# Kernel tuning notes

Measured on AMD Instinct MI355X. Metric: run time of the kernel, lower is better.

The kernel has to match this reference:

```python
import jax, jax.numpy as jnp
import numpy as np

H, D = 4, 8          # heads, per-head dim (hidden=32)
HID = 32
NA = 300_000         # addr nodes
NT = 300_000         # tx nodes
E_IN, E_OUT, E_SP = 1_000_000, 1_000_000, 500_000
NLAYERS = 4
NREL = 3


def setup_inputs() -> dict:
    key = jax.random.key(0)
    ks = iter(jax.random.split(key, 40))
    s = 0.1
    inp = {}
    inp['x_addr'] = jax.random.normal(next(ks), (NA, 53), jnp.float32)
    inp['x_tx'] = jax.random.normal(next(ks), (NT, 6), jnp.float32)
    inp['ei_input'] = jax.random.randint(next(ks), (2, E_IN), 0, NA, jnp.int32)   # addr -> tx
    inp['ei_output'] = jax.random.randint(next(ks), (2, E_OUT), 0, NT, jnp.int32)  # tx -> addr
    inp['ei_spent'] = jax.random.randint(next(ks), (2, E_SP), 0, NT, jnp.int32)   # tx -> tx
    # node encoders
    inp['enc_w_addr'] = jax.random.normal(next(ks), (53, HID), jnp.float32) * s
    inp['enc_b_addr'] = jnp.zeros((HID,), jnp.float32)
    inp['enc_w_tx'] = jax.random.normal(next(ks), (6, HID), jnp.float32) * s
    inp['enc_b_tx'] = jnp.zeros((HID,), jnp.float32)
    # layer norms (shared across layers as in the source)
    inp['ln_addr_g'] = jnp.ones((HID,), jnp.float32)
    inp['ln_addr_b'] = jnp.zeros((HID,), jnp.float32)
    inp['ln_tx_g'] = jnp.ones((HID,), jnp.float32)
    inp['ln_tx_b'] = jnp.zeros((HID,), jnp.float32)
    # 4 HANConv layers, params stacked on leading layer axis
    inp['proj_w_addr'] = jax.random.normal(next(ks), (NLAYERS, HID, HID), jnp.float32) * s
    inp['proj_b_addr'] = jnp.zeros((NLAYERS, HID), jnp.float32)
    inp['proj_w_tx'] = jax.random.normal(next(ks), (NLAYERS, HID, HID), jnp.float32) * s
    inp['proj_b_tx'] = jnp.zeros((NLAYERS, HID), jnp.float32)
    inp['att_src'] = jax.random.normal(next(ks), (NLAYERS, NREL, H, D), jnp.float32) * s
    inp['att_dst'] = jax.random.normal(next(ks), (NLAYERS, NREL, H, D), jnp.float32) * s
    inp['klin_w'] = jax.random.normal(next(ks), (NLAYERS, HID, HID), jnp.float32) * s
    inp['klin_b'] = jnp.zeros((NLAYERS, HID), jnp.float32)
    inp['q'] = jax.random.normal(next(ks), (NLAYERS, HID), jnp.float32) * s
    # output head
    inp['lin_w'] = jax.random.normal(next(ks), (HID, 2), jnp.float32) * s
    inp['lin_b'] = jnp.zeros((2,), jnp.float32)
    return inp


def _layernorm(x, g, b, eps=1e-5):
    m = x.mean(-1, keepdims=True)
    v = ((x - m) ** 2).mean(-1, keepdims=True)
    return (x - m) / jnp.sqrt(v + eps) * g + b


def _segment_softmax(alpha, idx, n):
    # alpha: [E, H]; numerically stable softmax over ragged segments (dst nodes)
    amax = jax.ops.segment_max(alpha, idx, num_segments=n)
    amax = jnp.where(jnp.isfinite(amax), amax, 0.0)
    ex = jnp.exp(alpha - amax[idx])
    den = jax.ops.segment_sum(ex, idx, num_segments=n)
    return ex / (den[idx] + 1e-16)


def _han_conv(xa, xt, ei_in, ei_out, ei_sp,
              pw_a, pb_a, pw_t, pb_t, a_src, a_dst, kw, kb, q):
    h_a = (xa @ pw_a + pb_a).reshape(-1, H, D)   # [NA,H,D]
    h_t = (xt @ pw_t + pb_t).reshape(-1, H, D)   # [NT,H,D]
    rels = [(h_a, h_t, ei_in, 0, 'tx'),     # ('addr','input','tx')
            (h_t, h_a, ei_out, 1, 'addr'),  # ('tx','output','addr')
            (h_t, h_t, ei_sp, 2, 'tx')]     # ('tx','spent_output','tx')
    outs = {'addr': [], 'tx': []}
    for hs, hd, ei, t, dname in rels:
        asrc = (hs * a_src[t]).sum(-1)   # [Ns,H]
        adst = (hd * a_dst[t]).sum(-1)   # [Nd,H]
        si, di = ei[0], ei[1]
        e = jax.nn.leaky_relu(asrc[si] + adst[di], negative_slope=0.2)  # [E,H]
        w = _segment_softmax(e, di, hd.shape[0])                        # [E,H]
        msg = hs[si] * w[:, :, None]                                    # [E,H,D]
        agg = jax.ops.segment_sum(msg, di, num_segments=hd.shape[0])
        outs[dname].append(jax.nn.relu(agg.reshape(-1, H * D)))
    def group(xs):
        out = jnp.stack(xs)                                   # [R,N,F]
        score = (q * jnp.tanh(out @ kw + kb).mean(1)).sum(-1)  # [R]
        attn = jax.nn.softmax(score)
        return (attn[:, None, None] * out).sum(0)
    return group(outs['addr']), group(outs['tx'])


def reference(x_addr, x_tx, ei_input, ei_output, ei_spent,
              enc_w_addr, enc_b_addr, enc_w_tx, enc_b_tx,
              ln_addr_g, ln_addr_b, ln_tx_g, ln_tx_b,
              proj_w_addr, proj_b_addr, proj_w_tx, proj_b_tx,
              att_src, att_dst, klin_w, klin_b, q,
              lin_w, lin_b):
    xa = jax.nn.relu(x_addr @ enc_w_addr + enc_b_addr)
    xt = jax.nn.relu(x_tx @ enc_w_tx + enc_b_tx)
    for l in range(NLAYERS):
        oa, ot = _han_conv(xa, xt, ei_input, ei_output, ei_spent,
                           proj_w_addr[l], proj_b_addr[l],
                           proj_w_tx[l], proj_b_tx[l],
                           att_src[l], att_dst[l],
                           klin_w[l], klin_b[l], q[l])
        xa = _layernorm(jax.nn.relu(oa) + xa, ln_addr_g, ln_addr_b)
        xt = _layernorm(jax.nn.relu(ot) + xt, ln_tx_g, ln_tx_b)
    return xa @ lin_w + lin_b
```

## Files before the change

### kernel.cpp

```cpp
#include <hip/hip_runtime.h>
#include <hip/hip_fp16.h>

#define NLAYERS 4
#define BSHIFT 10
#define CHUNK 4096

typedef _Float16 f16x8 __attribute__((ext_vector_type(8)));
typedef float f32x4 __attribute__((ext_vector_type(4)));

__global__ void zero_int_kernel(int* __restrict__ p, long n) {
    long i = (long)blockIdx.x * 256 + threadIdx.x;
    long stride = (long)gridDim.x * 256;
    for (; i < n; i += stride) p[i] = 0;
}

__device__ __forceinline__ float fast_tanh(float y) {
    y = fminf(fmaxf(y, -15.f), 15.f);
    float t = __expf(2.f * y);
    return (t - 1.f) / (t + 1.f);
}

__device__ __forceinline__ int edge_row(const int* ei_in, const int* ei_out, const int* ei_sp,
                                        int E_IN, int E_OUT, int E_SP, int NT, int NA,
                                        int e, int* src) {
    if (e < E_IN) { *src = ei_in[e]; return ei_in[E_IN + e]; }
    if (e < E_IN + E_OUT) { int i = e - E_IN; *src = ei_out[i]; return NT + ei_out[E_OUT + i]; }
    int i = e - E_IN - E_OUT; *src = ei_sp[i]; return NT + NA + ei_sp[E_SP + i];
}

__global__ void hist_kernel(const int* __restrict__ ei_in, const int* __restrict__ ei_out,
                            const int* __restrict__ ei_sp, int E_IN, int E_OUT, int E_SP,
                            int NT, int NA, int* __restrict__ deg, int E_TOT) {
    int e = blockIdx.x * 256 + threadIdx.x;
    if (e >= E_TOT) return;
    int s;
    int row = edge_row(ei_in, ei_out, ei_sp, E_IN, E_OUT, E_SP, NT, NA, e, &s);
    atomicAdd(&deg[row], 1);
}

__global__ void scatter_kernel(const int* __restrict__ ei_in, const int* __restrict__ ei_out,
                               const int* __restrict__ ei_sp, int E_IN, int E_OUT, int E_SP,
                               int NT, int NA, int* __restrict__ cursor, int* __restrict__ col,
                               int E_TOT) {
    int e = blockIdx.x * 256 + threadIdx.x;
    if (e >= E_TOT) return;
    int s;
    int row = edge_row(ei_in, ei_out, ei_sp, E_IN, E_OUT, E_SP, NT, NA, e, &s);
    int pos = atomicAdd(&cursor[row], 1);
    col[pos] = s;
}

__global__ void scan1_kernel(const int* __restrict__ deg, int* __restrict__ rowptr,
                             int* __restrict__ bsum, int n) {
    __shared__ int lds[256];
    int tid = threadIdx.x;
    int base = blockIdx.x * 1024;
    int v[4];
    int mysum = 0;
    #pragma unroll
    for (int j = 0; j < 4; j++) {
        int idx = base + tid * 4 + j;
        v[j] = (idx < n) ? deg[idx] : 0;
        mysum += v[j];
    }
    lds[tid] = mysum;
    __syncthreads();
    for (int off = 1; off < 256; off <<= 1) {
        int t = (tid >= off) ? lds[tid - off] : 0;
        __syncthreads();
        lds[tid] += t;
        __syncthreads();
    }
    int excl = lds[tid] - mysum;
    if (tid == 255) bsum[blockIdx.x] = lds[tid];
    int run = excl;
    #pragma unroll
    for (int j = 0; j < 4; j++) {
        int idx = base + tid * 4 + j;
        if (idx < n) rowptr[idx] = run;
        run += v[j];
    }
}

__global__ void scan2_kernel(int* __restrict__ bsum, int nb) {
    __shared__ int lds[1024];
    int tid = threadIdx.x;
    int v = (tid < nb) ? bsum[tid] : 0;
    lds[tid] = v;
    __syncthreads();
    for (int off = 1; off < 1024; off <<= 1) {
        int t = (tid >= off) ? lds[tid - off] : 0;
        __syncthreads();
        lds[tid] += t;
        __syncthreads();
    }
    if (tid < nb) bsum[tid] = lds[tid] - v;
}

__global__ void scan3_kernel(int* __restrict__ rowptr, const int* __restrict__ bsum,
                             int* __restrict__ cursor, int n, int E) {
    int i = blockIdx.x * 256 + threadIdx.x;
    if (i < n) {
        int r = rowptr[i] + bsum[i >> 10];
        rowptr[i] = r;
        cursor[i] = r;
    }
    if (i == 0) rowptr[n] = E;
}

__global__ void bucket_scatter_kernel(const int* __restrict__ ei_in, const int* __restrict__ ei_out,
                                      const int* __restrict__ ei_sp, int E_IN, int E_OUT, int E_SP,
                                      int NT, int NA, int* __restrict__ bcur,
                                      uint2* __restrict__ ebuf, int E_TOT, int nbuck, int cap) {
    __shared__ int lc[1024], lbase[1024], lcur[1024];
    int tid = threadIdx.x;
    int chunk0 = blockIdx.x * CHUNK;
    int chunkN = E_TOT - chunk0;
    if (chunkN > CHUNK) chunkN = CHUNK;
    if (chunkN <= 0) return;
    for (int i = tid; i < nbuck; i += 256) { lc[i] = 0; lcur[i] = 0; }
    __syncthreads();
    for (int i = tid; i < chunkN; i += 256) {
        int s;
        int row = edge_row(ei_in, ei_out, ei_sp, E_IN, E_OUT, E_SP, NT, NA, chunk0 + i, &s);
        atomicAdd(&lc[row >> BSHIFT], 1);
    }
    __syncthreads();
    for (int i = tid; i < nbuck; i += 256) if (lc[i]) lbase[i] = atomicAdd(&bcur[i], lc[i]);
    __syncthreads();
    for (int i = tid; i < chunkN; i += 256) {
        int s;
        int row = edge_row(ei_in, ei_out, ei_sp, E_IN, E_OUT, E_SP, NT, NA, chunk0 + i, &s);
        int b = row >> BSHIFT;
        int pos = lbase[b] + atomicAdd(&lcur[b], 1);
        if (pos < cap) ebuf[(size_t)b * cap + pos] = make_uint2((unsigned)row, (unsigned)s);
    }
}

__global__ void scanb_kernel(const int* __restrict__ bcur, int* __restrict__ boff,
                             int* __restrict__ rowptr, int nbuck, int cap, int NCAT) {
    __shared__ int lds[1024];
    int tid = threadIdx.x;
    int v = 0;
    if (tid < nbuck) { v = bcur[tid]; if (v > cap) v = cap; }
    lds[tid] = v;
    __syncthreads();
    for (int off = 1; off < 1024; off <<= 1) {
        int t = (tid >= off) ? lds[tid - off] : 0;
        __syncthreads();
        lds[tid] += t;
        __syncthreads();
    }
    if (tid < nbuck) boff[tid] = lds[tid] - v;
    if (tid == 1023) {
        boff[nbuck] = lds[1023];
        rowptr[NCAT] = lds[1023];
    }
}

__global__ void __launch_bounds__(256) bucket_csr_kernel(
    const uint2* __restrict__ ebuf, const int* __restrict__ boff,
    int* __restrict__ rowptr, int* __restrict__ col, int NCAT, int cap) {
    __shared__ int ldeg[1024];
    __shared__ int lsum[256];
    int tid = threadIdx.x;
    int b = blockIdx.x;
    int row0 = b << BSHIFT;
    int e0 = boff[b], e1 = boff[b + 1];
    int cnt = e1 - e0;
    const uint2* src = ebuf + (size_t)b * cap;
    for (int i = tid; i < 1024; i += 256) ldeg[i] = 0;
    __syncthreads();
    for (int i = tid; i < cnt; i += 256)
        atomicAdd(&ldeg[src[i].x - (unsigned)row0], 1);
    __syncthreads();
    int bidx = tid * 4;
    int v0 = ldeg[bidx], v1 = ldeg[bidx + 1], v2 = ldeg[bidx + 2], v3 = ldeg[bidx + 3];
    int mysum = v0 + v1 + v2 + v3;
    lsum[tid] = mysum;
    __syncthreads();
    for (int off = 1; off < 256; off <<= 1) {
        int t = (tid >= off) ? lsum[tid - off] : 0;
        __syncthreads();
        lsum[tid] += t;
        __syncthreads();
    }
    int run = e0 + lsum[tid] - mysum;
    int vv[4] = {v0, v1, v2, v3};
    #pragma unroll
    for (int j = 0; j < 4; j++) {
        int r = bidx + j;
        if (row0 + r < NCAT) rowptr[row0 + r] = run;
        ldeg[r] = run;
        run += vv[j];
    }
    __syncthreads();
    for (int i = tid; i < cnt; i += 256) {
        uint2 p = src[i];
        int pos = atomicAdd(&ldeg[p.x - (unsigned)row0], 1);
        col[pos] = (int)p.y;
    }
}

__global__ void __launch_bounds__(256) encproj_addr_kernel(
    const float* __restrict__ x,
    const float* __restrict__ We, const float* __restrict__ be,
    const float* __restrict__ Wp, const float* __restrict__ bp,
    const float* __restrict__ a0, const float* __restrict__ a1,
    float* __restrict__ xa, __half* __restrict__ h,
    __half* __restrict__ o0, float* __restrict__ o1,
    int n, int gpb) {
    __shared__ __align__(16) float lds_t[4][16][36];
    __shared__ float sx[4][16 * 57];
    int tid = threadIdx.x;
    int wave = tid >> 6, lane = tid & 63;
    int colid = lane & 15, kgrp = lane >> 4;
    int fbase = kgrp * 8;

    f16x8 bE00, bE01, bE10, bE11;
    #pragma unroll
    for (int j = 0; j < 8; j++) {
        int k0 = fbase + j;
        int k1 = 32 + fbase + j;
        bE00[j] = (_Float16)We[k0 * 32 + colid];
        bE01[j] = (_Float16)We[k0 * 32 + 16 + colid];
        float w10 = (k1 < 53) ? We[k1 * 32 + colid] : 0.f;
        float w11 = (k1 < 53) ? We[k1 * 32 + 16 + colid] : 0.f;
        bE10[j] = (_Float16)w10;
        bE11[j] = (_Float16)w11;
    }
    float beC0 = be[colid], beC1 = be[16 + colid];

    f16x8 bP0, bP1;
    #pragma unroll
    for (int j = 0; j < 8; j++) {
        bP0[j] = (_Float16)Wp[(fbase + j) * 32 + colid];
        bP1[j] = (_Float16)Wp[(fbase + j) * 32 + 16 + colid];
    }
    float bpC0 = bp[colid], bpC1 = bp[16 + colid];

    float va0[8], va1[8];
    #pragma unroll
    for (int j = 0; j < 8; j++) { va0[j] = a0[fbase + j]; va1[j] = a1[fbase + j]; }

    float (*tp)[36] = lds_t[wave];
    float* sxw = sx[wave];
    int blockBase = blockIdx.x * gpb * 64;
    for (int gi = 0; gi < gpb; gi++) {
        int node0 = blockBase + gi * 64 + wave * 16;
        int node = node0 + colid;
        bool valid = node < n;
        int nn = n - node0;
        if (nn > 16) nn = 16;
        if (nn < 0) nn = 0;
        int elems = nn * 53;
        for (int i = lane; i < elems; i += 64) {
            int r = i / 53, c = i - r * 53;
            sxw[r * 57 + c] = x[(size_t)node0 * 53 + i];
        }
        f16x8 af0, af1;
        #pragma unroll
        for (int j = 0; j < 8; j++) {
            af0[j] = (_Float16)sxw[colid * 57 + fbase + j];
            int kk = 32 + fbase + j;
            float v1 = (kk < 53) ? sxw[colid * 57 + kk] : 0.f;
            af1[j] = (_Float16)v1;
        }
        f32x4 c0 = {0.f, 0.f, 0.f, 0.f};
        f32x4 c1 = {0.f, 0.f, 0.f, 0.f};
        c0 = __builtin_amdgcn_mfma_f32_16x16x32_f16(af0, bE00, c0, 0, 0, 0);
        c0 = __builtin_amdgcn_mfma_f32_16x16x32_f16(af1, bE10, c0, 0, 0, 0);
        c1 = __builtin_amdgcn_mfma_f32_16x16x32_f16(af0, bE01, c1, 0, 0, 0);
        c1 = __builtin_amdgcn_mfma_f32_16x16x32_f16(af1, bE11, c1, 0, 0, 0);
        #pragma unroll
        for (int r = 0; r < 4; r++) {
            c0[r] = fmaxf(c0[r] + beC0, 0.f);
            c1[r] = fmaxf(c1[r] + beC1, 0.f);
        }
        #pragma unroll
        for (int r = 0; r < 4; r++) {
            int row = kgrp * 4 + r;
            tp[row][colid] = c0[r];
            tp[row][16 + colid] = c1[r];
        }
        float4 xlo = *(const float4*)&tp[colid][fbase];
        float4 xhi = *(const float4*)&tp[colid][fbase + 4];
        float xe[8] = {xlo.x, xlo.y, xlo.z, xlo.w, xhi.x, xhi.y, xhi.z, xhi.w};
        if (valid) {
            size_t basep = (size_t)node * 32 + fbase;
            *(float4*)(xa + basep) = xlo;
            *(float4*)(xa + basep + 4) = xhi;
        }
        f16x8 af;
        #pragma unroll
        for (int j = 0; j < 8; j++) af[j] = (_Float16)xe[j];
        f32x4 p0 = {0.f, 0.f, 0.f, 0.f};
        f32x4 p1 = {0.f, 0.f, 0.f, 0.f};
        p0 = __builtin_amdgcn_mfma_f32_16x16x32_f16(af, bP0, p0, 0, 0, 0);
        p1 = __builtin_amdgcn_mfma_f32_16x16x32_f16(af, bP1, p1, 0, 0, 0);
        #pragma unroll
        for (int r = 0; r < 4; r++) { p0[r] += bpC0; p1[r] += bpC1; }
        #pragma unroll
        for (int r = 0; r < 4; r++) {
            int row = kgrp * 4 + r;
            tp[row][colid] = p0[r];
            tp[row][16 + colid] = p1[r];
        }
        float4 hlo = *(const float4*)&tp[colid][fbase];
        float4 hhi = *(const float4*)&tp[colid][fbase + 4];
        float hv[8] = {hlo.x, hlo.y, hlo.z, hlo.w, hhi.x, hhi.y, hhi.z, hhi.w};
        if (valid) {
            float4 hout;
            __half2* hp2 = (__half2*)&hout;
            hp2[0] = __floats2half2_rn(hv[0], hv[1]);
            hp2[1] = __floats2half2_rn(hv[2], hv[3]);
            hp2[2] = __floats2half2_rn(hv[4], hv[5]);
            hp2[3] = __floats2half2_rn(hv[6], hv[7]);
            *(float4*)(h + (size_t)node * 32 + fbase) = hout;
            float d0 = 0.f, d1 = 0.f;
            #pragma unroll
            for (int j = 0; j < 8; j++) {
                d0 += hv[j] * va0[j];
                d1 += hv[j] * va1[j];
            }
            size_t oidx = (size_t)node * 4 + kgrp;
            o0[oidx] = __float2half(d0);
            o1[oidx] = d1;
        }
    }
}

__global__ void __launch_bounds__(256) encproj_tx_kernel(
    const float* __restrict__ x,
    const float* __restrict__ We, const float* __restrict__ be,
    const float* __restrict__ Wp, const float* __restrict__ bp,
    const float* __restrict__ a0, const float* __restrict__ a1,
    const float* __restrict__ a2, const float* __restrict__ a3,
    float* __restrict__ xt, __half* __restrict__ h,
    __half* __restrict__ o0, float* __restrict__ o1,
    __half* __restrict__ o2, float* __restrict__ o3,
    int n, int gpb) {
    __shared__ __align__(16) float lds_t[4][16][36];
    int tid = threadIdx.x;
    int wave = tid >> 6, lane = tid & 63;
    int colid = lane & 15, kgrp = lane >> 4;
    int fbase = kgrp * 8;

    f16x8 bE0, bE1;
    #pragma unroll
    for (int j = 0; j < 8; j++) {
        int k = fbase + j;
        float w0 = (k < 6) ? We[k * 32 + colid] : 0.f;
        float w1 = (k < 6) ? We[k * 32 + 16 + colid] : 0.f;
        bE0[j] = (_Float16)w0;
        bE1[j] = (_Float16)w1;
    }
    float beC0 = be[colid], beC1 = be[16 + colid];

    f16x8 bP0, bP1;
    #pragma unroll
    for (int j = 0; j < 8; j++) {
        bP0[j] = (_Float16)Wp[(fbase + j) * 32 + colid];
        bP1[j] = (_Float16)Wp[(fbase + j) * 32 + 16 + colid];
    }
    float bpC0 = bp[colid], bpC1 = bp[16 + colid];

    float va0[8], va1[8], va2[8], va3[8];
    #pragma unroll
    for (int j = 0; j < 8; j++) {
        va0[j] = a0[fbase + j]; va1[j] = a1[fbase + j];
        va2[j] = a2[fbase + j]; va3[j] = a3[fbase + j];
    }

    float (*tp)[36] = lds_t[wave];
    int blockBase = blockIdx.x * gpb * 64;
    for (int gi = 0; gi < gpb; gi++) {
        int node = blockBase + gi * 64 + wave * 16 + colid;
        bool valid = node < n;
        f16x8 af0;
        #pragma unroll
        for (int j = 0; j < 8; j++) {
            int k = fbase + j;
            float xv = 0.f;
            if (k < 6 && valid) xv = x[(size_t)node * 6 + k];
            af0[j] = (_Float16)xv;
        }
        f32x4 c0 = {0.f, 0.f, 0.f, 0.f};
        f32x4 c1 = {0.f, 0.f, 0.f, 0.f};
        c0 = __builtin_amdgcn_mfma_f32_16x16x32_f16(af0, bE0, c0, 0, 0, 0);
        c1 = __builtin_amdgcn_mfma_f32_16x16x32_f16(af0, bE1, c1, 0, 0, 0);
        #pragma unroll
        for (int r = 0; r < 4; r++) {
            c0[r] = fmaxf(c0[r] + beC0, 0.f);
            c1[r] = fmaxf(c1[r] + beC1, 0.f);
        }
        #pragma unroll
        for (int r = 0; r < 4; r++) {
            int row = kgrp * 4 + r;
            tp[row][colid] = c0[r];
            tp[row][16 + colid] = c1[r];
        }
        float4 xlo = *(const float4*)&tp[colid][fbase];
        float4 xhi = *(const float4*)&tp[colid][fbase + 4];
        float xe[8] = {xlo.x, xlo.y, xlo.z, xlo.w, xhi.x, xhi.y, xhi.z, xhi.w};
        if (valid) {
            size_t basep = (size_t)node * 32 + fbase;
            *(float4*)(xt + basep) = xlo;
            *(float4*)(xt + basep + 4) = xhi;
        }
        f16x8 af;
        #pragma unroll
        for (int j = 0; j < 8; j++) af[j] = (_Float16)xe[j];
        f32x4 p0 = {0.f, 0.f, 0.f, 0.f};
        f32x4 p1 = {0.f, 0.f, 0.f, 0.f};
        p0 = __builtin_amdgcn_mfma_f32_16x16x32_f16(af, bP0, p0, 0, 0, 0);
        p1 = __builtin_amdgcn_mfma_f32_16x16x32_f16(af, bP1, p1, 0, 0, 0);
        #pragma unroll
        for (int r = 0; r < 4; r++) { p0[r] += bpC0; p1[r] += bpC1; }
        #pragma unroll
        for (int r = 0; r < 4; r++) {
            int row = kgrp * 4 + r;
            tp[row][colid] = p0[r];
            tp[row][16 + colid] = p1[r];
        }
        float4 hlo = *(const float4*)&tp[colid][fbase];
        float4 hhi = *(const float4*)&tp[colid][fbase + 4];
        float hv[8] = {hlo.x, hlo.y, hlo.z, hlo.w, hhi.x, hhi.y, hhi.z, hhi.w};
        if (valid) {
            float4 hout;
            __half2* hp2 = (__half2*)&hout;
            hp2[0] = __floats2half2_rn(hv[0], hv[1]);
            hp2[1] = __floats2half2_rn(hv[2], hv[3]);
            hp2[2] = __floats2half2_rn(hv[4], hv[5]);
            hp2[3] = __floats2half2_rn(hv[6], hv[7]);
            *(float4*)(h + (size_t)node * 32 + fbase) = hout;
            float d0 = 0.f, d1 = 0.f, d2 = 0.f, d3 = 0.f;
            #pragma unroll
            for (int j = 0; j < 8; j++) {
                d0 += hv[j] * va0[j];
                d1 += hv[j] * va1[j];
                d2 += hv[j] * va2[j];
                d3 += hv[j] * va3[j];
            }
            size_t oidx = (size_t)node * 4 + kgrp;
            o0[oidx] = __float2half(d0);
            o1[oidx] = d1;
            o2[oidx] = __float2half(d2);
            o3[oidx] = d3;
        }
    }
}

__global__ void agg_all_kernel(
    const int* __restrict__ rowptr, const int* __restrict__ col,
    const __half* __restrict__ h_a, const __half* __restrict__ h_t,
    const __half* __restrict__ asrc0, const float* __restrict__ adst0,
    const __half* __restrict__ asrc1, const float* __restrict__ adst1,
    const __half* __restrict__ asrc2, const float* __restrict__ adst2,
    __half* __restrict__ agg_t0, __half* __restrict__ agg_a, __half* __restrict__ agg_t2,
    const float* __restrict__ kw, const float* __restrict__ kb, const float* __restrict__ q,
    float* __restrict__ scoreOut, int NT, int NA, int mode, int nRows) {
    __shared__ float sW[1024];
    __shared__ float sb[32];
    __shared__ float sq[32];
    __shared__ float sScore[2];
    int tid = threadIdx.x;
    bool doScore = (mode != 2);
    if (doScore) {
        for (int i = tid; i < 1024; i += 256) sW[i] = kw[i];
        if (tid < 32) { sb[tid] = kb[tid]; sq[tid] = q[tid]; }
        if (tid < 2) sScore[tid] = 0.f;
        __syncthreads();
    }
    int lane = tid & 7;
    int head = lane >> 1;
    int f0 = lane * 4;
    long stride = (long)gridDim.x * 32;
    for (long gi = (long)blockIdx.x * 32 + (tid >> 3); gi < (long)nRows; gi += stride) {
        int row;
        if (mode == 0) row = (int)gi;
        else if (mode == 1) row = (gi < NT) ? (int)gi : (int)(gi + NA);
        else row = NT + (int)gi;
        int rel, dst;
        const __half* h; const __half* asrc; const float* adp; __half* agg;
        if (row < NT)           { rel = 0; dst = row;           h = h_a; asrc = asrc0; adp = adst0; agg = agg_t0; }
        else if (row < NT + NA) { rel = 1; dst = row - NT;      h = h_t; asrc = asrc1; adp = adst1; agg = agg_a; }
        else                    { rel = 2; dst = row - NT - NA; h = h_t; asrc = asrc2; adp = adst2; agg = agg_t2; }
        float ad = adp[dst * 4 + head];
        int e0 = rowptr[row], e1 = rowptr[row + 1];
        __half2 acc0 = __floats2half2_rn(0.f, 0.f);
        __half2 acc1 = acc0;
        float den = 0.f;
        for (int e = e0; e < e1; e += 4) {
            int s0 = col[e];
            int s1 = (e + 1 < e1) ? col[e + 1] : s0;
            int s2 = (e + 2 < e1) ? col[e + 2] : s0;
            int s3 = (e + 3 < e1) ? col[e + 3] : s0;
            float as0 = __half2float(asrc[s0 * 4 + head]);
            float as1 = __half2float(asrc[s1 * 4 + head]);
            float as2 = __half2float(asrc[s2 * 4 + head]);
            float as3 = __half2float(asrc[s3 * 4 + head]);
            float2 r0 = *(const float2*)(h + s0 * 32 + f0);
            float2 r1 = *(const float2*)(h + s1 * 32 + f0);
            float2 r2 = *(const float2*)(h + s2 * 32 + f0);
            float2 r3 = *(const float2*)(h + s3 * 32 + f0);
            float t0 = as0 + ad; t0 = t0 > 0.f ? t0 : 0.2f * t0;
            float t1 = as1 + ad; t1 = t1 > 0.f ? t1 : 0.2f * t1;
            float t2 = as2 + ad; t2 = t2 > 0.f ? t2 : 0.2f * t2;
            float t3 = as3 + ad; t3 = t3 > 0.f ? t3 : 0.2f * t3;
            float ex0 = __expf(t0);
            float ex1 = (e + 1 < e1) ? __expf(t1) : 0.f;
            float ex2 = (e + 2 < e1) ? __expf(t2) : 0.f;
            float ex3 = (e + 3 < e1) ? __expf(t3) : 0.f;
            den += (ex0 + ex1) + (ex2 + ex3);
            __half2 eh0 = __float2half2_rn(ex0), eh1 = __float2half2_rn(ex1);
            __half2 eh2 = __float2half2_rn(ex2), eh3 = __float2half2_rn(ex3);
            acc0 = __hfma2(eh0, *(__half2*)&r0.x, acc0);
            acc1 = __hfma2(eh0, *(__half2*)&r0.y, acc1);
            acc0 = __hfma2(eh1, *(__half2*)&r1.x, acc0);
            acc1 = __hfma2(eh1, *(__half2*)&r1.y, acc1);
            acc0 = __hfma2(eh2, *(__half2*)&r2.x, acc0);
            acc1 = __hfma2(eh2, *(__half2*)&r2.y, acc1);
            acc0 = __hfma2(eh3, *(__half2*)&r3.x, acc0);
            acc1 = __hfma2(eh3, *(__half2*)&r3.y, acc1);
        }
        float r = 1.f / (den + 1e-16f);
        float2 a0 = __half22float2(acc0), a1 = __half22float2(acc1);
        float v0 = a0.x * r, v1 = a0.y * r, v2 = a1.x * r, v3 = a1.y * r;
        float2 opack;
        __half2 o0 = __floats2half2_rn(v0, v1), o1 = __floats2half2_rn(v2, v3);
        opack.x = *(float*)&o0; opack.y = *(float*)&o1;
        *(float2*)(agg + dst * 32 + f0) = opack;
        if (doScore && rel != 1) {
            float rv0 = fmaxf(v0, 0.f), rv1 = fmaxf(v1, 0.f);
            float rv2 = fmaxf(v2, 0.f), rv3 = fmaxf(v3, 0.f);
            float y0 = sb[f0], y1 = sb[f0 + 1], y2 = sb[f0 + 2], y3 = sb[f0 + 3];
            #pragma unroll
            for (int g = 0; g < 8; g++) {
                float c0 = __shfl(rv0, g, 8);
                float c1 = __shfl(rv1, g, 8);
                float c2 = __shfl(rv2, g, 8);
                float c3 = __shfl(rv3, g, 8);
                int kb4 = g * 4;
                y0 += c0 * sW[(kb4 + 0) * 32 + f0] + c1 * sW[(kb4 + 1) * 32 + f0]
                    + c2 * sW[(kb4 + 2) * 32 + f0] + c3 * sW[(kb4 + 3) * 32 + f0];
                y1 += c0 * sW[(kb4 + 0) * 32 + f0 + 1] + c1 * sW[(kb4 + 1) * 32 + f0 + 1]
                    + c2 * sW[(kb4 + 2) * 32 + f0 + 1] + c3 * sW[(kb4 + 3) * 32 + f0 + 1];
                y2 += c0 * sW[(kb4 + 0) * 32 + f0 + 2] + c1 * sW[(kb4 + 1) * 32 + f0 + 2]
                    + c2 * sW[(kb4 + 2) * 32 + f0 + 2] + c3 * sW[(kb4 + 3) * 32 + f0 + 2];
                y3 += c0 * sW[(kb4 + 0) * 32 + f0 + 3] + c1 * sW[(kb4 + 1) * 32 + f0 + 3]
                    + c2 * sW[(kb4 + 2) * 32 + f0 + 3] + c3 * sW[(kb4 + 3) * 32 + f0 + 3];
            }
            float sacc = sq[f0] * fast_tanh(y0) + sq[f0 + 1] * fast_tanh(y1)
                       + sq[f0 + 2] * fast_tanh(y2) + sq[f0 + 3] * fast_tanh(y3);
            #pragma unroll
            for (int m = 1; m < 8; m <<= 1) sacc += __shfl_xor(sacc, m, 8);
            if (lane == 0) atomicAdd(&sScore[rel == 2 ? 1 : 0], sacc);
        }
    }
    if (doScore) {
        __syncthreads();
        if (tid < 2) unsafeAtomicAdd(scoreOut + tid, sScore[tid]);
    }
}

__global__ void __launch_bounds__(256) combineproj_kernel(
    const __half* __restrict__ agg_a, const __half* __restrict__ agg_t0, const __half* __restrict__ agg_t2,
    float* __restrict__ xa, float* __restrict__ xt,
    const float* __restrict__ ln_ag, const float* __restrict__ ln_ab,
    const float* __restrict__ ln_tg, const float* __restrict__ ln_tb,
    const float* __restrict__ scores, float invNT,
    const float* __restrict__ Wa, const float* __restrict__ Ba,
    const float* __restrict__ Wt, const float* __restrict__ Bt,
    const float* __restrict__ as0, const float* __restrict__ ad1,
    const float* __restrict__ as1, const float* __restrict__ ad0,
    const float* __restrict__ as2, const float* __restrict__ ad2,
    __half* __restrict__ h_a, __half* __restrict__ h_t,
    __half* __restrict__ o_as0, float* __restrict__ o_ad1,
    __half* __restrict__ o_as1, float* __restrict__ o_ad0,
    __half* __restrict__ o_as2, float* __restrict__ o_ad2,
    int NA_, int NT_, int nbAcp, int gpb, int lastProj) {
    __shared__ __align__(16) float lds_t[4][16][36];
    int tid = threadIdx.x;
    int wave = tid >> 6;
    int lane = tid & 63;
    int colid = lane & 15;
    int kgrp = lane >> 4;
    int fbase = kgrp * 8;

    bool isA = blockIdx.x < (unsigned)nbAcp;
    const float* W = isA ? Wa : Wt;
    const float* Bp = isA ? Ba : Bt;
    int n = isA ? NA_ : NT_;

    f16x8 bf0, bf1;
    #pragma unroll
    for (int j = 0; j < 8; j++) {
        bf0[j] = (_Float16)W[(fbase + j) * 32 + colid];
        bf1[j] = (_Float16)W[(fbase + j) * 32 + 16 + colid];
    }
    float bp0 = Bp[colid], bp1 = Bp[16 + colid];

    const float* lng = isA ? ln_ag : ln_tg;
    const float* lnb = isA ? ln_ab : ln_tb;
    float g[8], bb[8];
    #pragma unroll
    for (int j = 0; j < 8; j++) { g[j] = lng[fbase + j]; bb[j] = lnb[fbase + j]; }

    float va0[8], va1[8], va2[8], va3[8];
    if (isA) {
        #pragma unroll
        for (int j = 0; j < 8; j++) { va0[j] = as0[fbase + j]; va1[j] = ad1[fbase + j]; }
    } else {
        #pragma unroll
        for (int j = 0; j < 8; j++) {
            va0[j] = as1[fbase + j]; va1[j] = ad0[fbase + j];
            va2[j] = as2[fbase + j]; va3[j] = ad2[fbase + j];
        }
    }

    float wsem0 = 0.f, wsem2 = 0.f;
    if (!isA) {
        float s0 = scores[0] * invNT, s2 = scores[1] * invNT;
        float mx = fmaxf(s0, s2);
        float e0 = __expf(s0 - mx), e2 = __expf(s2 - mx);
        float inv_s = 1.f / (e0 + e2);
        wsem0 = e0 * inv_s; wsem2 = e2 * inv_s;
    }

    float (*tp)[36] = lds_t[wave];
    int blockBase = (isA ? (int)blockIdx.x : (int)blockIdx.x - nbAcp) * gpb * 64;
    for (int gi = 0; gi < gpb; gi++) {
        int node = blockBase + gi * 64 + wave * 16 + colid;
        bool valid = node < n;
        float v[8];
        if (valid) {
            size_t base = (size_t)node * 32 + fbase;
            float4 xlo, xhi;
            if (isA) {
                xlo = *(const float4*)(xa + base);
                xhi = *(const float4*)(xa + base + 4);
                float4 ar = *(const float4*)(agg_a + base);
                const __half2* ah2 = (const __half2*)&ar;
                float2 f0 = __half22float2(ah2[0]);
                float2 f1 = __half22float2(ah2[1]);
                float2 f2 = __half22float2(ah2[2]);
                float2 f3 = __half22float2(ah2[3]);
                float av[8] = {f0.x, f0.y, f1.x, f1.y, f2.x, f2.y, f3.x, f3.y};
                float xv[8] = {xlo.x, xlo.y, xlo.z, xlo.w, xhi.x, xhi.y, xhi.z, xhi.w};
                #pragma unroll
                for (int j = 0; j < 8; j++) v[j] = fmaxf(av[j], 0.f) + xv[j];
            } else {
                xlo = *(const float4*)(xt + base);
                xhi = *(const float4*)(xt + base + 4);
                float4 a0r = *(const float4*)(agg_t0 + base);
                float4 a2r = *(const float4*)(agg_t2 + base);
                const __half2* a0h = (const __half2*)&a0r;
                const __half2* a2h = (const __half2*)&a2r;
                float xv[8] = {xlo.x, xlo.y, xlo.z, xlo.w, xhi.x, xhi.y, xhi.z, xhi.w};
                #pragma unroll
                for (int j = 0; j < 4; j++) {
                    float2 p0 = __half22float2(a0h[j]);
                    float2 p2 = __half22float2(a2h[j]);
                    float c0 = wsem0 * fmaxf(p0.x, 0.f) + wsem2 * fmaxf(p2.x, 0.f);
                    float c1 = wsem0 * fmaxf(p0.y, 0.f) + wsem2 * fmaxf(p2.y, 0.f);
                    v[2 * j]     = fmaxf(c0, 0.f) + xv[2 * j];
                    v[2 * j + 1] = fmaxf(c1, 0.f) + xv[2 * j + 1];
                }
            }
        } else {
            #pragma unroll
            for (int j = 0; j < 8; j++) v[j] = 0.f;
        }
        float s = 0.f;
        #pragma unroll
        for (int j = 0; j < 8; j++) s += v[j];
        s += __shfl_xor(s, 16, 64);
        s += __shfl_xor(s, 32, 64);
        float m = s * 0.03125f;
        float d[8], vv = 0.f;
        #pragma unroll
        for (int j = 0; j < 8; j++) { d[j] = v[j] - m; vv += d[j] * d[j]; }
        vv += __shfl_xor(vv, 16, 64);
        vv += __shfl_xor(vv, 32, 64);
        float inv = 1.f / sqrtf(vv * 0.03125f + 1e-5f);
        float ln[8];
        #pragma unroll
        for (int j = 0; j < 8; j++) ln[j] = d[j] * inv * g[j] + bb[j];

        if (valid && (isA || !lastProj)) {
            float* xp = isA ? xa : xt;
            size_t base = (size_t)node * 32 + fbase;
            *(float4*)(xp + base)     = make_float4(ln[0], ln[1], ln[2], ln[3]);
            *(float4*)(xp + base + 4) = make_float4(ln[4], ln[5], ln[6], ln[7]);
        }

        f16x8 af;
        #pragma unroll
        for (int j = 0; j < 8; j++) af[j] = (_Float16)ln[j];
        f32x4 c0 = {0.f, 0.f, 0.f, 0.f};
        f32x4 c1 = {0.f, 0.f, 0.f, 0.f};
        c0 = __builtin_amdgcn_mfma_f32_16x16x32_f16(af, bf0, c0, 0, 0, 0);
        c1 = __builtin_amdgcn_mfma_f32_16x16x32_f16(af, bf1, c1, 0, 0, 0);
        #pragma unroll
        for (int r = 0; r < 4; r++) { c0[r] += bp0; c1[r] += bp1; }

        #pragma unroll
        for (int r = 0; r < 4; r++) {
            int row = kgrp * 4 + r;
            tp[row][colid] = c0[r];
            tp[row][16 + colid] = c1[r];
        }
        float4 hlo = *(const float4*)&tp[colid][fbase];
        float4 hhi = *(const float4*)&tp[colid][fbase + 4];
        float hv[8] = {hlo.x, hlo.y, hlo.z, hlo.w, hhi.x, hhi.y, hhi.z, hhi.w};

        bool writeH = (!isA || !lastProj);
        if (valid && writeH) {
            float4 hout;
            __half2* hp2 = (__half2*)&hout;
            hp2[0] = __floats2half2_rn(hv[0], hv[1]);
            hp2[1] = __floats2half2_rn(hv[2], hv[3]);
            hp2[2] = __floats2half2_rn(hv[4], hv[5]);
            hp2[3] = __floats2half2_rn(hv[6], hv[7]);
            __half* hp = isA ? h_a : h_t;
            *(float4*)(hp + (size_t)node * 32 + fbase) = hout;
        }

        if (valid) {
            size_t oidx = (size_t)node * 4 + kgrp;
            if (isA) {
                if (!lastProj) {
                    float ds = 0.f;
                    #pragma unroll
                    for (int j = 0; j < 8; j++) ds += hv[j] * va0[j];
                    o_as0[oidx] = __float2half(ds);
                }
                float dd = 0.f;
                #pragma unroll
                for (int j = 0; j < 8; j++) dd += hv[j] * va1[j];
                o_ad1[oidx] = dd;
            } else {
                float d0 = 0.f;
                #pragma unroll
                for (int j = 0; j < 8; j++) d0 += hv[j] * va0[j];
                o_as1[oidx] = __float2half(d0);
                if (!lastProj) {
                    float d1 = 0.f, d2 = 0.f, d3 = 0.f;
                    #pragma unroll
                    for (int j = 0; j < 8; j++) {
                        d1 += hv[j] * va1[j];
                        d2 += hv[j] * va2[j];
                        d3 += hv[j] * va3[j];
                    }
                    o_ad0[oidx] = d1;
                    o_as2[oidx] = __float2half(d2);
                    o_ad2[oidx] = d3;
                }
            }
        }
    }
}

__global__ void combine_final_kernel(const __half* __restrict__ agg_a, const float* __restrict__ xa,
                                     const float* __restrict__ g, const float* __restrict__ bt,
                                     const float* __restrict__ lw, const float* __restrict__ lb,
                                     float* __restrict__ out, int n) {
    int tid = threadIdx.x;
    int local = tid >> 5, f = tid & 31;
    int node = blockIdx.x * 8 + local;
    if (node >= n) return;
    float a = __half2float(agg_a[(size_t)node * 32 + f]);
    float v = fmaxf(a, 0.f) + xa[(size_t)node * 32 + f];
    float m = v;
    #pragma unroll
    for (int mask = 1; mask < 32; mask <<= 1) m += __shfl_xor(m, mask, 64);
    m *= (1.f / 32.f);
    float d = v - m;
    float var = d * d;
    #pragma unroll
    for (int mask = 1; mask < 32; mask <<= 1) var += __shfl_xor(var, mask, 64);
    var *= (1.f / 32.f);
    float inv = 1.f / sqrtf(var + 1e-5f);
    float ln = d * inv * g[f] + bt[f];
    float p0 = ln * lw[f * 2 + 0];
    float p1 = ln * lw[f * 2 + 1];
    #pragma unroll
    for (int mask = 1; mask < 32; mask <<= 1) {
        p0 += __shfl_xor(p0, mask, 64);
        p1 += __shfl_xor(p1, mask, 64);
    }
    if (f == 0) {
        out[(size_t)node * 2 + 0] = p0 + lb[0];
        out[(size_t)node * 2 + 1] = p1 + lb[1];
    }
}

extern "C" void kernel_launch(void* const* d_in, const int* in_sizes, int n_in,
                              void* d_out, int out_size, void* d_ws, size_t ws_size,
                              hipStream_t stream) {
    const float* x_addr = (const float*)d_in[0];
    const float* x_tx   = (const float*)d_in[1];
    const int* ei_in    = (const int*)d_in[2];
    const int* ei_out   = (const int*)d_in[3];
    const int* ei_sp    = (const int*)d_in[4];
    const float* enc_w_addr = (const float*)d_in[5];
    const float* enc_b_addr = (const float*)d_in[6];
    const float* enc_w_tx   = (const float*)d_in[7];
    const float* enc_b_tx   = (const float*)d_in[8];
    const float* ln_ag = (const float*)d_in[9];
    const float* ln_ab = (const float*)d_in[10];
    const float* ln_tg = (const float*)d_in[11];
    const float* ln_tb = (const float*)d_in[12];
    const float* pw_a = (const float*)d_in[13];
    const float* pb_a = (const float*)d_in[14];
    const float* pw_t = (const float*)d_in[15];
    const float* pb_t = (const float*)d_in[16];
    const float* att_src = (const float*)d_in[17];
    const float* att_dst = (const float*)d_in[18];
    const float* klw = (const float*)d_in[19];
    const float* klb = (const float*)d_in[20];
    const float* qv  = (const float*)d_in[21];
    const float* lin_w = (const float*)d_in[22];
    const float* lin_b = (const float*)d_in[23];
    float* out = (float*)d_out;

    const int NA = in_sizes[0] / 53;
    const int NT = in_sizes[1] / 6;
    const int E_IN = in_sizes[2] / 2;
    const int E_OUT = in_sizes[3] / 2;
    const int E_SP = in_sizes[4] / 2;
    const int E_TOT = E_IN + E_OUT + E_SP;
    const int NCAT = NT + NA + NT;
    const int NBUCK = (NCAT + (1 << BSHIFT) - 1) >> BSHIFT;

    size_t off = 0;
    float* base = (float*)d_ws;
    auto alloc = [&](size_t nfloats) {
        float* p = base + off;
        off += (nfloats + 63) & ~(size_t)63;
        return p;
    };
    float* xa      = alloc((size_t)NA * 32);
    float* xt      = alloc((size_t)NT * 32);
    float* agg_a_f = alloc((size_t)NA * 16);
    float* agg_t0f = alloc((size_t)NT * 16);
    float* agg_t2f = alloc((size_t)NT * 16);
    float* h_t_f   = alloc((size_t)NT * 16);
    float* asrc0a  = alloc((size_t)NA * 2);
    float* adst1a  = alloc((size_t)NA * 4);
    float* asrc1t  = alloc((size_t)NT * 2);
    float* adst0t  = alloc((size_t)NT * 4);
    float* asrc2t  = alloc((size_t)NT * 2);
    float* adst2t  = alloc((size_t)NT * 4);
    int* rowptrAll = (int*)alloc((size_t)NCAT + 64);
    int* colAll    = (int*)alloc((size_t)E_TOT);
    size_t tmp_span = (((size_t)NCAT + 63) & ~(size_t)63) + 1088 + 64 + 1024;
    int* tmp       = (int*)alloc((size_t)NCAT);
    int* bsum      = (int*)alloc(1088);
    float* scores  = alloc(64);
    int* bcur      = (int*)alloc(1024);
    int* boff      = (int*)alloc(1088);

    size_t ha_floats = (((size_t)NA * 16) + 63) & ~(size_t)63;
    bool roomy = ((off + ha_floats) * sizeof(float)) <= ws_size;
    float* h_a_f = roomy ? alloc((size_t)NA * 16) : agg_a_f;

    int avgb = (int)(((long)E_TOT << BSHIFT) / (long)NCAT);
    int cap = ((avgb + avgb / 4 + 256) + 255) & ~255;
    size_t ebuf_floats = (size_t)NBUCK * (size_t)cap * 2;
    bool canBucket = (NBUCK <= 1024) &&
                     (((off + ebuf_floats + 64) * sizeof(float)) <= ws_size);
    uint2* ebuf = canBucket ? (uint2*)alloc(ebuf_floats) : nullptr;

    __half* agg_a  = (__half*)agg_a_f;
    __half* agg_t0 = (__half*)agg_t0f;
    __half* agg_t2 = (__half*)agg_t2f;
    __half* h_t    = (__half*)h_t_f;
    __half* h_a    = (__half*)h_a_f;
    __half* has0   = (__half*)asrc0a;
    __half* has1   = (__half*)asrc1t;
    __half* has2   = (__half*)asrc2t;

    dim3 blk(256);
    const int GPB_E = 4;
    const int GPB_C = 4;
    int nbA8 = (NA + 7) / 8;
    int nbAe = (NA + 64 * GPB_E - 1) / (64 * GPB_E);
    int nbTe = (NT + 64 * GPB_E - 1) / (64 * GPB_E);
    int nbAcp = (NA + 64 * GPB_C - 1) / (64 * GPB_C);
    int nbTcp = (NT + 64 * GPB_C - 1) / (64 * GPB_C);
    int nbE = (E_TOT + 255) / 256;
    int nbScan = (NCAT + 1023) / 1024;

    if (canBucket) {
        int nbChunk = (E_TOT + CHUNK - 1) / CHUNK;
        zero_int_kernel<<<8, blk, 0, stream>>>((int*)scores, 64 + 1024);
        bucket_scatter_kernel<<<nbChunk, blk, 0, stream>>>(
            ei_in, ei_out, ei_sp, E_IN, E_OUT, E_SP, NT, NA, bcur, ebuf, E_TOT, NBUCK, cap);
        scanb_kernel<<<1, 1024, 0, stream>>>(bcur, boff, rowptrAll, NBUCK, cap, NCAT);
        bucket_csr_kernel<<<NBUCK, blk, 0, stream>>>(ebuf, boff, rowptrAll, colAll, NCAT, cap);
    } else {
        zero_int_kernel<<<2048, blk, 0, stream>>>(tmp, (long)tmp_span);
        hist_kernel<<<nbE, blk, 0, stream>>>(ei_in, ei_out, ei_sp, E_IN, E_OUT, E_SP, NT, NA, tmp, E_TOT);
        scan1_kernel<<<nbScan, blk, 0, stream>>>(tmp, rowptrAll, bsum, NCAT);
        scan2_kernel<<<1, 1024, 0, stream>>>(bsum, nbScan);
        scan3_kernel<<<(NCAT + 255) / 256, blk, 0, stream>>>(rowptrAll, bsum, tmp, NCAT, E_TOT);
        scatter_kernel<<<nbE, blk, 0, stream>>>(ei_in, ei_out, ei_sp, E_IN, E_OUT, E_SP, NT, NA, tmp, colAll, E_TOT);
    }

    encproj_addr_kernel<<<nbAe, blk, 0, stream>>>(
        x_addr, enc_w_addr, enc_b_addr, pw_a, pb_a,
        att_src + 0 * 32, att_dst + 1 * 32,
        xa, h_a, has0, adst1a, NA, GPB_E);
    encproj_tx_kernel<<<nbTe, blk, 0, stream>>>(
        x_tx, enc_w_tx, enc_b_tx, pw_t, pb_t,
        att_src + 1 * 32, att_dst + 0 * 32, att_src + 2 * 32, att_dst + 2 * 32,
        xt, h_t, has1, adst0t, has2, adst2t, NT, GPB_E);

    auto agg_launch = [&](int mode, int nRows, const float* kw, const float* kb,
                          const float* q, float* sc) {
        int blocks = (nRows + 31) / 32;
        if (blocks > 2048) blocks = 2048;
        agg_all_kernel<<<blocks, blk, 0, stream>>>(
            rowptrAll, colAll, h_a, h_t,
            has0, adst0t, has1, adst1a, has2, adst2t,
            agg_t0, agg_a, agg_t2, kw, kb, q, sc, NT, NA, mode, nRows);
    };

    for (int l = 0; l < NLAYERS; l++) {
        bool last = (l == NLAYERS - 1);
        const float* kw = klw + l * 1024;
        const float* kb = klb + l * 32;
        const float* q  = qv + l * 32;
        float* sc = scores + 2 * l;
        if (!last) {
            if (roomy) {
                agg_launch(0, NCAT, kw, kb, q, sc);
            } else {
                agg_launch(1, 2 * NT, kw, kb, q, sc);
                agg_launch(2, NA, kw, kb, q, sc);
            }
            int lp = l + 1;
            combineproj_kernel<<<nbAcp + nbTcp, blk, 0, stream>>>(
                agg_a, agg_t0, agg_t2, xa, xt,
                ln_ag, ln_ab, ln_tg, ln_tb,
                sc, 1.0f / (float)NT,
                pw_a + lp * 1024, pb_a + lp * 32, pw_t + lp * 1024, pb_t + lp * 32,
                att_src + (lp * 3 + 0) * 32, att_dst + (lp * 3 + 1) * 32,
                att_src + (lp * 3 + 1) * 32, att_dst + (lp * 3 + 0) * 32,
                att_src + (lp * 3 + 2) * 32, att_dst + (lp * 3 + 2) * 32,
                h_a, h_t,
                has0, adst1a, has1, adst0t, has2, adst2t,
                NA, NT, nbAcp, GPB_C, lp == 3 ? 1 : 0);
        } else {
            agg_launch(2, NA, kw, kb, q, sc);
            combine_final_kernel<<<nbA8, blk, 0, stream>>>(agg_a, xa, ln_ag, ln_ab,
                                                           lin_w, lin_b, out, NA);
        }
    }
}
```

Baseline: 770.8 us.

## Split semantic-attention scoring out of aggregation into MFMA-based score kernel

Removes the per-row 32x32 klin matvec, tanh and score reduction from the edge aggregation kernel, dropping its shared-memory weight staging and sync. A new score_tx_kernel reads the fp16 aggregated tx outputs back and computes tanh(x@kw+kb)·q with 16x16x32 f16 MFMA instructions, reducing via wave shuffles and atomics. This makes the gather kernel lighter and lowers its register and LDS footprint, at the cost of an extra launch and a re-read of both tx aggregation buffers each layer. The relu is now applied in half precision before the matmul, and kw is rounded to fp16.

After: 788.9 us. 1.02x slower.

```diff
diff --git a/kernel.cpp b/kernel.cpp
--- a/kernel.cpp
+++ b/kernel.cpp
@@ -18,6 +18,11 @@
     y = fminf(fmaxf(y, -15.f), 15.f);
     float t = __expf(2.f * y);
     return (t - 1.f) / (t + 1.f);
+}
+
+__device__ __forceinline__ __half2 h2relu(__half2 v) {
+    float2 f = __half22float2(v);
+    return __floats2half2_rn(fmaxf(f.x, 0.f), fmaxf(f.y, 0.f));
 }
 
 __device__ __forceinline__ int edge_row(const int* ei_in, const int* ei_out, const int* ei_sp,
@@ -451,27 +456,15 @@
     }
 }
 
-__global__ void agg_all_kernel(
+__global__ void __launch_bounds__(256) agg_all_kernel(
     const int* __restrict__ rowptr, const int* __restrict__ col,
     const __half* __restrict__ h_a, const __half* __restrict__ h_t,
     const __half* __restrict__ asrc0, const float* __restrict__ adst0,
     const __half* __restrict__ asrc1, const float* __restrict__ adst1,
     const __half* __restrict__ asrc2, const float* __restrict__ adst2,
     __half* __restrict__ agg_t0, __half* __restrict__ agg_a, __half* __restrict__ agg_t2,
-    const float* __restrict__ kw, const float* __restrict__ kb, const float* __restrict__ q,
-    float* __restrict__ scoreOut, int NT, int NA, int mode, int nRows) {
-    __shared__ float sW[1024];
-    __shared__ float sb[32];
-    __shared__ float sq[32];
-    __shared__ float sScore[2];
-    int tid = threadIdx.x;
-    bool doScore = (mode != 2);
-    if (doScore) {
-        for (int i = tid; i < 1024; i += 256) sW[i] = kw[i];
-        if (tid < 32) { sb[tid] = kb[tid]; sq[tid] = q[tid]; }
-        if (tid < 2) sScore[tid] = 0.f;
-        __syncthreads();
-    }
+    int NT, int NA, int mode, int nRows) {
+    int tid = threadIdx.x;
     int lane = tid & 7;
     int head = lane >> 1;
     int f0 = lane * 4;
@@ -481,11 +474,11 @@
         if (mode == 0) row = (int)gi;
         else if (mode == 1) row = (gi < NT) ? (int)gi : (int)(gi + NA);
         else row = NT + (int)gi;
-        int rel, dst;
+        int dst;
         const __half* h; const __half* asrc; const float* adp; __half* agg;
-        if (row < NT)           { rel = 0; dst = row;           h = h_a; asrc = asrc0; adp = adst0; agg = agg_t0; }
-        else if (row < NT + NA) { rel = 1; dst = row - NT;      h = h_t; asrc = asrc1; adp = adst1; agg = agg_a; }
-        else                    { rel = 2; dst = row - NT - NA; h = h_t; asrc = asrc2; adp = adst2; agg = agg_t2; }
+        if (row < NT)           { dst = row;           h = h_a; asrc = asrc0; adp = adst0; agg = agg_t0; }
+        else if (row < NT + NA) { dst = row - NT;      h = h_t; asrc = asrc1; adp = adst1; agg = agg_a; }
+        else                    { dst = row - NT - NA; h = h_t; asrc = asrc2; adp = adst2; agg = agg_t2; }
         float ad = adp[dst * 4 + head];
         int e0 = rowptr[row], e1 = rowptr[row + 1];
         __half2 acc0 = __floats2half2_rn(0.f, 0.f);
@@ -531,37 +524,75 @@
         __half2 o0 = __floats2half2_rn(v0, v1), o1 = __floats2half2_rn(v2, v3);
         opack.x = *(float*)&o0; opack.y = *(float*)&o1;
         *(float2*)(agg + dst * 32 + f0) = opack;
-        if (doScore && rel != 1) {
-            float rv0 = fmaxf(v0, 0.f), rv1 = fmaxf(v1, 0.f);
-            float rv2 = fmaxf(v2, 0.f), rv3 = fmaxf(v3, 0.f);
-            float y0 = sb[f0], y1 = sb[f0 + 1], y2 = sb[f0 + 2], y3 = sb[f0 + 3];
+    }
+}
+
+__global__ void __launch_bounds__(256) score_tx_kernel(
+    const __half* __restrict__ agg_t0, const __half* __restrict__ agg_t2,
+    const float* __restrict__ kw, const float* __restrict__ kb,
+    const float* __restrict__ q, float* __restrict__ scoreOut, int n, int gpb) {
+    __shared__ float sS[2];
+    int tid = threadIdx.x;
+    int wave = tid >> 6, lane = tid & 63;
+    int colid = lane & 15, kgrp = lane >> 4;
+    int fbase = kgrp * 8;
+    if (tid < 2) sS[tid] = 0.f;
+    __syncthreads();
+
+    f16x8 bK0, bK1;
+    #pragma unroll
+    for (int j = 0; j < 8; j++) {
+        bK0[j] = (_Float16)kw[(fbase + j) * 32 + colid];
+        bK1[j] = (_Float16)kw[(fbase + j) * 32 + 16 + colid];
+    }
+    float kb0 = kb[colid], kb1 = kb[16 + colid];
+    float q0 = q[colid], q1 = q[16 + colid];
+
+    float s0acc = 0.f, s2acc = 0.f;
+    int blockBase = blockIdx.x * gpb * 64;
+    for (int gi = 0; gi < gpb; gi++) {
+        int grp0 = blockBase + gi * 64 + wave * 16;
+        int nodeA = grp0 + colid;
+        bool validA = nodeA < n;
+        f16x8 af0 = {}, af2 = {};
+        if (validA) {
+            float4 r0 = *(const float4*)(agg_t0 + (size_t)nodeA * 32 + fbase);
+            float4 r2 = *(const float4*)(agg_t2 + (size_t)nodeA * 32 + fbase);
+            __half2* h0 = (__half2*)&r0;
+            __half2* h2 = (__half2*)&r2;
             #pragma unroll
-            for (int g = 0; g < 8; g++) {
-                float c0 = __shfl(rv0, g, 8);
-                float c1 = __shfl(rv1, g, 8);
-                float c2 = __shfl(rv2, g, 8);
-                float c3 = __shfl(rv3, g, 8);
-                int kb4 = g * 4;
-                y0 += c0 * sW[(kb4 + 0) * 32 + f0] + c1 * sW[(kb4 + 1) * 32 + f0]
-                    + c2 * sW[(kb4 + 2) * 32 + f0] + c3 * sW[(kb4 + 3) * 32 + f0];
-                y1 += c0 * sW[(kb4 + 0) * 32 + f0 + 1] + c1 * sW[(kb4 + 1) * 32 + f0 + 1]
-                    + c2 * sW[(kb4 + 2) * 32 + f0 + 1] + c3 * sW[(kb4 + 3) * 32 + f0 + 1];
-                y2 += c0 * sW[(kb4 + 0) * 32 + f0 + 2] + c1 * sW[(kb4 + 1) * 32 + f0 + 2]
-                    + c2 * sW[(kb4 + 2) * 32 + f0 + 2] + c3 * sW[(kb4 + 3) * 32 + f0 + 2];
-                y3 += c0 * sW[(kb4 + 0) * 32 + f0 + 3] + c1 * sW[(kb4 + 1) * 32 + f0 + 3]
-                    + c2 * sW[(kb4 + 2) * 32 + f0 + 3] + c3 * sW[(kb4 + 3) * 32 + f0 + 3];
+            for (int j = 0; j < 4; j++) {
+                h0[j] = h2relu(h0[j]);
+                h2[j] = h2relu(h2[j]);
             }
-            float sacc = sq[f0] * fast_tanh(y0) + sq[f0 + 1] * fast_tanh(y1)
-                       + sq[f0 + 2] * fast_tanh(y2) + sq[f0 + 3] * fast_tanh(y3);
-            #pragma unroll
-            for (int m = 1; m < 8; m <<= 1) sacc += __shfl_xor(sacc, m, 8);
-            if (lane == 0) atomicAdd(&sScore[rel == 2 ? 1 : 0], sacc);
-        }
-    }
-    if (doScore) {
-        __syncthreads();
-        if (tid < 2) unsafeAtomicAdd(scoreOut + tid, sScore[tid]);
-    }
+            af0 = *(f16x8*)&r0;
+            af2 = *(f16x8*)&r2;
+        }
+        f32x4 c00 = {0.f, 0.f, 0.f, 0.f}, c01 = {0.f, 0.f, 0.f, 0.f};
+        f32x4 c20 = {0.f, 0.f, 0.f, 0.f}, c21 = {0.f, 0.f, 0.f, 0.f};
+        c00 = __builtin_amdgcn_mfma_f32_16x16x32_f16(af0, bK0, c00, 0, 0, 0);
+        c01 = __builtin_amdgcn_mfma_f32_16x16x32_f16(af0, bK1, c01, 0, 0, 0);
+        c20 = __builtin_amdgcn_mfma_f32_16x16x32_f16(af2, bK0, c20, 0, 0, 0);
+        c21 = __builtin_amdgcn_mfma_f32_16x16x32_f16(af2, bK1, c21, 0, 0, 0);
+        #pragma unroll
+        for (int r = 0; r < 4; r++) {
+            if (grp0 + kgrp * 4 + r < n) {
+                s0acc += q0 * fast_tanh(c00[r] + kb0) + q1 * fast_tanh(c01[r] + kb1);
+                s2acc += q0 * fast_tanh(c20[r] + kb0) + q1 * fast_tanh(c21[r] + kb1);
+            }
+        }
+    }
+    #pragma unroll
+    for (int m = 1; m < 64; m <<= 1) {
+        s0acc += __shfl_xor(s0acc, m, 64);
+        s2acc += __shfl_xor(s2acc, m, 64);
+    }
+    if (lane == 0) {
+        atomicAdd(&sS[0], s0acc);
+        atomicAdd(&sS[1], s2acc);
+    }
+    __syncthreads();
+    if (tid < 2) unsafeAtomicAdd(scoreOut + tid, sS[tid]);
 }
 
 __global__ void __launch_bounds__(256) combineproj_kernel(
@@ -885,11 +916,13 @@
     dim3 blk(256);
     const int GPB_E = 4;
     const int GPB_C = 4;
+    const int GPB_S = 8;
     int nbA8 = (NA + 7) / 8;
     int nbAe = (NA + 64 * GPB_E - 1) / (64 * GPB_E);
     int nbTe = (NT + 64 * GPB_E - 1) / (64 * GPB_E);
     int nbAcp = (NA + 64 * GPB_C - 1) / (64 * GPB_C);
     int nbTcp = (NT + 64 * GPB_C - 1) / (64 * GPB_C);
+    int nbTs  = (NT + 64 * GPB_S - 1) / (64 * GPB_S);
     int nbE = (E_TOT + 255) / 256;
     int nbScan = (NCAT + 1023) / 1024;
 
@@ -918,14 +951,13 @@
         att_src + 1 * 32, att_dst + 0 * 32, att_src + 2 * 32, att_dst + 2 * 32,
         xt, h_t, has1, adst0t, has2, adst2t, NT, GPB_E);
 
-    auto agg_launch = [&](int mode, int nRows, const float* kw, const float* kb,
-                          const float* q, float* sc) {
+    auto agg_launch = [&](int mode, int nRows) {
         int blocks = (nRows + 31) / 32;
         if (blocks > 2048) blocks = 2048;
         agg_all_kernel<<<blocks, blk, 0, stream>>>(
             rowptrAll, colAll, h_a, h_t,
             has0, adst0t, has1, adst1a, has2, adst2t,
-            agg_t0, agg_a, agg_t2, kw, kb, q, sc, NT, NA, mode, nRows);
+            agg_t0, agg_a, agg_t2, NT, NA, mode, nRows);
     };
 
     for (int l = 0; l < NLAYERS; l++) {
@@ -936,11 +968,12 @@
         float* sc = scores + 2 * l;
         if (!last) {
             if (roomy) {
-                agg_launch(0, NCAT, kw, kb, q, sc);
+                agg_launch(0, NCAT);
             } else {
-                agg_launch(1, 2 * NT, kw, kb, q, sc);
-                agg_launch(2, NA, kw, kb, q, sc);
+                agg_launch(1, 2 * NT);
+                agg_launch(2, NA);
             }
+            score_tx_kernel<<<nbTs, blk, 0, stream>>>(agg_t0, agg_t2, kw, kb, q, sc, NT, GPB_S);
             int lp = l + 1;
             combineproj_kernel<<<nbAcp + nbTcp, blk, 0, stream>>>(
                 agg_a, agg_t0, agg_t2, xa, xt,
@@ -954,7 +987,7 @@
                 has0, adst1a, has1, adst0t, has2, adst2t,
                 NA, NT, nbAcp, GPB_C, lp == 3 ? 1 : 0);
         } else {
-            agg_launch(2, NA, kw, kb, q, sc);
+            agg_launch(2, NA);
             combine_final_kernel<<<nbA8, blk, 0, stream>>>(agg_a, xa, ln_ag, ln_ab,
                                                            lin_w, lin_b, out, NA);
         }
```
